# Kernel optimization log

Measured on AMD Instinct MI355X. Metric: run time of the kernel, lower is better.

Reference implementation:

```python
import jax, jax.numpy as jnp
import numpy as np

B, S = 2, 2048
DIM_IN, DIM_OUT, NUM_HEADS, DIM_QK = 1024, 128, 16, 128


def setup_inputs() -> dict:
    key = jax.random.key(0)
    k0, k1, k2, k3 = jax.random.split(key, 4)
    x = jax.random.normal(k0, (B, S, DIM_IN), jnp.float32)
    mask = jax.random.bernoulli(k1, 0.1, (B, S))  # True = masked-out token
    # xavier-normal-ish scales (exact init values are irrelevant for correctness)
    std_in = float(np.sqrt(2.0 / (NUM_HEADS * DIM_QK + DIM_IN * DIM_QK)))
    proj_in = jax.random.normal(k2, (DIM_IN, NUM_HEADS, 2 * DIM_QK + DIM_OUT), jnp.float32) * std_in
    v_bias = jnp.zeros((NUM_HEADS, DIM_OUT), jnp.float32)
    std_out = float(np.sqrt(2.0 / (DIM_OUT * DIM_OUT + NUM_HEADS * DIM_OUT)))
    proj_out = jax.random.normal(k3, (NUM_HEADS, DIM_OUT, DIM_OUT), jnp.float32) * std_out
    proj_out_bias = jnp.zeros((DIM_OUT,), jnp.float32)
    return {"x": x, "mask": mask, "proj_in": proj_in, "v_bias": v_bias,
            "proj_out": proj_out, "proj_out_bias": proj_out_bias}


def _rotary(t):
    # t: [z, s, h, d]; GPT-NeoX style rotary as in the torch Rotary module
    d = t.shape[-1]
    half = -(-d // 2)  # ceil(d/2), matches torch.arange(0,-1,-2/d)
    freq_half = 10000.0 ** (jnp.arange(half, dtype=jnp.float32) * (-2.0 / d))
    freq = jnp.concatenate([freq_half, freq_half[: half - d % 2]])  # length d
    pos = jnp.arange(t.shape[1], dtype=jnp.float32)
    ang = pos[:, None] * freq[None, :]             # [s, d]
    cos = jnp.cos(ang)[None, :, None, :]
    sin = jnp.sin(ang)[None, :, None, :]
    x1, x2 = jnp.split(t, 2, axis=-1)
    rot = jnp.concatenate([-x2, x1], axis=-1)
    return t * cos + rot * sin


def _inf_cube(t):
    return t ** 3


def reference(x, mask, proj_in, v_bias, proj_out, proj_out_bias):
    qkv = jnp.einsum('zki,iho->zkho', x, proj_in)
    q, k, v = jnp.split(qkv, [DIM_QK, 2 * DIM_QK], axis=-1)
    q = _rotary(q)
    k = _rotary(k)
    scores = jnp.einsum('zqha,zkha->zqkh', q, k) / jnp.sqrt(jnp.float32(DIM_QK))
    # dual mask: row (query) OR column (key) masked -> -inf
    m = jnp.logical_or(mask[:, :, None, None], mask[:, None, :, None])  # [z,q,k,1]
    scores = jnp.where(m, -jnp.inf, scores)
    attn = jnp.nan_to_num(jax.nn.softmax(scores, axis=2))  # softmax over k; nan rows -> 0
    o = jnp.einsum('zqkh,zkhx->zqhx', attn, v + v_bias[None, None])
    out = jnp.einsum('zqhx,hxy->zqy', _inf_cube(o), proj_out) + proj_out_bias[None, None]
    return _inf_cube(out)
```

## Files before the change

kernel.cpp:

```cpp
#include <hip/hip_runtime.h>
#include <math.h>

#define BZ 2
#define SQ 2048
#define DIN 1024
#define HH 16
#define NT 6144
#define MROWS 4096
#define KOUT 2048
#define KSPLIT 8

typedef unsigned short u16t;
typedef unsigned int u32t;
typedef __attribute__((ext_vector_type(8))) short bf16x8;
typedef __attribute__((ext_vector_type(4))) float f32x4;

__device__ __forceinline__ float cubef(float x) { return x * x * x; }

__device__ __forceinline__ u16t f2bf(float f) {
    u32t b = __float_as_uint(f);
    b += 0x7FFFu + ((b >> 16) & 1u);
    return (u16t)(b >> 16);
}
__device__ __forceinline__ float bf2f(u16t u) { return __uint_as_float(((u32t)u) << 16); }
__device__ __forceinline__ u32t pk2(float a, float b) {
    return (u32t)f2bf(a) | ((u32t)f2bf(b) << 16);
}

#if __has_builtin(__builtin_amdgcn_exp2f)
#define EXP2(x) __builtin_amdgcn_exp2f(x)
#else
#define EXP2(x) exp2f(x)
#endif

__device__ __forceinline__ void load_lds16(const void* g, void* l) {
    __builtin_amdgcn_global_load_lds((const __attribute__((address_space(1))) void*)g,
                                     (__attribute__((address_space(3))) void*)l, 16, 0, 0);
}

__global__ __launch_bounds__(256) void prep_all(const float* __restrict__ x,
                                                u16t* __restrict__ xb,
                                                float* __restrict__ tab,
                                                const float* __restrict__ W,
                                                u16t* __restrict__ Th) {
    __shared__ float tile[64][68];
    const int bx = blockIdx.x;
    const int t = threadIdx.x;

    if (bx < 2048) {
        const size_t idx = ((size_t)bx * 256 + t) * 8;
        float4 f0 = *(const float4*)&x[idx];
        float4 f1 = *(const float4*)&x[idx + 4];
        u32t h[4];
        h[0] = pk2(f0.x, f0.y); h[1] = pk2(f0.z, f0.w);
        h[2] = pk2(f1.x, f1.y); h[3] = pk2(f1.z, f1.w);
        *(uint4*)&xb[idx] = *(uint4*)&h[0];
    } else if (bx < 2560) {
        const int idx = (bx - 2048) * 256 + t;
        const int s = idx >> 6, d = idx & 63;
        float f = expf(-0.14391156831212788f * (float)d);
        float sn, cs;
        sincosf((float)s * f, &sn, &cs);
        ((float2*)tab)[idx] = make_float2(cs, sn);
    } else {
        const int idx = bx - 2560;
        const int n0 = (idx % 96) * 64;
        const int k0 = (idx / 96) * 64;
        {
            const int r = t >> 4, c = (t & 15) * 4;
            #pragma unroll
            for (int p = 0; p < 4; p++) {
                float4 v = *(const float4*)&W[(size_t)(k0 + r + p * 16) * NT + n0 + c];
                *(float4*)&tile[r + p * 16][c] = v;
            }
        }
        __syncthreads();
        const int nr = t >> 2;
        const int kc = (t & 3) * 16;
        u32t hi[8];
        #pragma unroll
        for (int j = 0; j < 8; j++)
            hi[j] = pk2(tile[kc + 2 * j][nr], tile[kc + 2 * j + 1][nr]);
        size_t ob = (size_t)(n0 + nr) * DIN + k0 + kc;
        *(uint4*)&Th[ob]     = *(uint4*)&hi[0];
        *(uint4*)&Th[ob + 8] = *(uint4*)&hi[4];
    }
}

__global__ __launch_bounds__(256) void transpose_w2(const float* __restrict__ W,
                                                    u16t* __restrict__ Th) {
    __shared__ float tile[64][68];
    const int n0 = blockIdx.x * 64;
    const int k0 = blockIdx.y * 64;
    const int t = threadIdx.x;
    {
        const int r = t >> 4, c = (t & 15) * 4;
        #pragma unroll
        for (int p = 0; p < 4; p++) {
            float4 v = *(const float4*)&W[(size_t)(k0 + r + p * 16) * 128 + n0 + c];
            *(float4*)&tile[r + p * 16][c] = v;
        }
    }
    __syncthreads();
    const int nr = t >> 2;
    const int kc = (t & 3) * 16;
    u32t hi[8];
    #pragma unroll
    for (int j = 0; j < 8; j++)
        hi[j] = pk2(tile[kc + 2 * j][nr], tile[kc + 2 * j + 1][nr]);
    size_t ob = (size_t)(n0 + nr) * KOUT + k0 + kc;
    *(uint4*)&Th[ob]     = *(uint4*)&hi[0];
    *(uint4*)&Th[ob + 8] = *(uint4*)&hi[4];
}

#define QSC 0.12751744f

__global__ __launch_bounds__(256) void gemm_qkv9(const u16t* __restrict__ Ah,
                                                 const u16t* __restrict__ Bh,
                                                 const float* __restrict__ vb,
                                                 const float* __restrict__ ropetab,
                                                 u16t* __restrict__ QB,
                                                 u16t* __restrict__ KB,
                                                 u16t* __restrict__ VTh) {
    __shared__ __align__(16) u16t smem[17408];

    const int t = threadIdx.x;
    const int lane = t & 63, wid = t >> 6;
    const int quad = lane >> 4, l15 = lane & 15;
    const int wm = (wid & 1) * 64;
    const int wn = (wid >> 1) * 64;

    const int f = blockIdx.y * 48 + blockIdx.x;
    const int L = (f & 7) * 192 + (f >> 3);
    const int rect = L / 48, rrem = L - rect * 48;
    const int tileI = (rect & 7) * 6 + rrem % 6;
    const int rowIdx = (rect >> 3) * 8 + rrem / 6;
    const int h = tileI / 3, t3 = tileI - h * 3;
    const int colBase = tileI * 128;
    const int rowBase = rowIdx * 128;
    const int sm = t & 127;
    const int skh = t >> 7;

    f32x4 acc[4][4];
    #pragma unroll
    for (int i = 0; i < 4; i++)
        #pragma unroll
        for (int j = 0; j < 4; j++) acc[i][j] = (f32x4){0.f, 0.f, 0.f, 0.f};

    const u16t* aPtr = Ah + (size_t)(rowBase + sm) * DIN + skh * 16;
    const u16t* bPtr = Bh + (size_t)(colBase + sm) * DIN + skh * 16;
    const int swoff = skh * 2048 + sm * 8;

    uint4 a0 = *(const uint4*)(aPtr);
    uint4 a1 = *(const uint4*)(aPtr + 8);
    uint4 b0 = *(const uint4*)(bPtr);
    uint4 b1 = *(const uint4*)(bPtr + 8);

    for (int it = 0; it < 32; it++) {
        const int buf = it & 1;
        const int ab = buf * 4096, bb_ = 8192 + buf * 4096;
        *(uint4*)(&smem[ab + swoff])         = a0;
        *(uint4*)(&smem[ab + swoff + 1024])  = a1;
        *(uint4*)(&smem[bb_ + swoff])        = b0;
        *(uint4*)(&smem[bb_ + swoff + 1024]) = b1;
        __syncthreads();
        {
            const int k0 = (it < 31) ? (it + 1) * 32 : it * 32;
            a0 = *(const uint4*)(aPtr + k0);
            a1 = *(const uint4*)(aPtr + k0 + 8);
            b0 = *(const uint4*)(bPtr + k0);
            b1 = *(const uint4*)(bPtr + k0 + 8);
        }
        bf16x8 ah[4], bh[4];
        #pragma unroll
        for (int mt = 0; mt < 4; mt++)
            ah[mt] = *(const bf16x8*)&smem[ab + quad * 1024 + (wm + mt * 16 + l15) * 8];
        #pragma unroll
        for (int nt = 0; nt < 4; nt++)
            bh[nt] = *(const bf16x8*)&smem[bb_ + quad * 1024 + (wn + nt * 16 + l15) * 8];
        __builtin_amdgcn_s_setprio(1);
        #pragma unroll
        for (int mt = 0; mt < 4; mt++)
            #pragma unroll
            for (int nt = 0; nt < 4; nt++)
                acc[mt][nt] = __builtin_amdgcn_mfma_f32_16x16x32_bf16(ah[mt], bh[nt], acc[mt][nt], 0, 0, 0);
        __builtin_amdgcn_s_setprio(0);
    }
    __syncthreads();

    const int z = rowBase >> 11;
    const int s0local = rowBase & 2047;
    const size_t zh = (size_t)(z * 16 + h);
    u16t* tl = smem;

    if (t3 == 2) {
        #pragma unroll
        for (int nt = 0; nt < 4; nt++) {
            float bbv = vb[h * 128 + wn + nt * 16 + l15];
            #pragma unroll
            for (int mt = 0; mt < 4; mt++)
                #pragma unroll
                for (int r = 0; r < 4; r++)
                    tl[(wm + mt * 16 + quad * 4 + r) * 136 + wn + nt * 16 + l15] =
                        f2bf(acc[mt][nt][r] + bbv);
        }
    } else {
        #pragma unroll
        for (int nt = 0; nt < 4; nt++)
            #pragma unroll
            for (int mt = 0; mt < 4; mt++)
                #pragma unroll
                for (int r = 0; r < 4; r++)
                    tl[(wm + mt * 16 + quad * 4 + r) * 136 + wn + nt * 16 + l15] =
                        f2bf(acc[mt][nt][r]);
    }
    __syncthreads();

    if (t3 != 2) {
        u16t* dstQK = (t3 ? KB : QB) + zh * 262144;
        const float sc = t3 ? 1.0f : QSC;
        const int rr = t >> 2;
        const int ch = (t & 3) << 4;
        #pragma unroll
        for (int half = 0; half < 2; half++) {
            const int row = rr + half * 64;
            const int s = s0local + row;
            const u16t* trow = &tl[row * 136];
            uint4 X1  = *(const uint4*)&trow[ch];
            uint4 X1b = *(const uint4*)&trow[ch + 8];
            uint4 X2  = *(const uint4*)&trow[ch + 64];
            uint4 X2b = *(const uint4*)&trow[ch + 72];
            u32t A_[8] = {X1.x, X1.y, X1.z, X1.w, X1b.x, X1b.y, X1b.z, X1b.w};
            u32t B_[8] = {X2.x, X2.y, X2.z, X2.w, X2b.x, X2b.y, X2b.z, X2b.w};
            u32t OA[8], OB[8];
            const float4* tb = (const float4*)&ropetab[(size_t)s * 128 + ch * 2];
            #pragma unroll
            for (int p = 0; p < 8; p++) {
                float4 tt = tb[p];
                float cs0 = tt.x * sc, sn0 = tt.y * sc;
                float cs1 = tt.z * sc, sn1 = tt.w * sc;
                float x1a = bf2f((u16t)(A_[p] & 0xFFFFu)), x1b = bf2f((u16t)(A_[p] >> 16));
                float x2a = bf2f((u16t)(B_[p] & 0xFFFFu)), x2b = bf2f((u16t)(B_[p] >> 16));
                OA[p] = pk2(x1a * cs0 - x2a * sn0, x1b * cs1 - x2b * sn1);
                OB[p] = pk2(x2a * cs0 + x1a * sn0, x2b * cs1 + x1b * sn1);
            }
            u16t* d0 = dstQK + (size_t)s * 128 + ch;
            *(uint4*)d0        = make_uint4(OA[0], OA[1], OA[2], OA[3]);
            *(uint4*)(d0 + 8)  = make_uint4(OA[4], OA[5], OA[6], OA[7]);
            *(uint4*)(d0 + 64) = make_uint4(OB[0], OB[1], OB[2], OB[3]);
            *(uint4*)(d0 + 72) = make_uint4(OB[4], OB[5], OB[6], OB[7]);
        }
    } else {
        u16t* dstV = VTh + zh * 262144 + (size_t)(s0local >> 5) * 4096;
        const int d = t & 127;
        const int g0 = t >> 7;
        #pragma unroll
        for (int gg = 0; gg < 2; gg++) {
            const int g = g0 + 2 * gg;
            const u16t* col = &tl[(g * 32) * 136 + d];
            u32t H[16];
            #pragma unroll
            for (int m = 0; m < 16; m++) {
                u32t lo = col[m * 136];
                u32t hi = col[(m + 16) * 136];
                H[m] = lo | (hi << 16);
            }
            u16t* dv = dstV + (size_t)g * 4096 + d * 32;
            *(uint4*)&dv[0]  = *(uint4*)&H[0];
            *(uint4*)&dv[8]  = *(uint4*)&H[4];
            *(uint4*)&dv[16] = *(uint4*)&H[8];
            *(uint4*)&dv[24] = *(uint4*)&H[12];
        }
    }
}

__global__ __launch_bounds__(256, 2) void attn_kernel9(const u16t* __restrict__ QB,
                                                       const u16t* __restrict__ KB,
                                                       const u16t* __restrict__ VTh,
                                                       const int* __restrict__ mask,
                                                       u16t* __restrict__ O3b) {
    const int blk = blockIdx.x;
    const int qt = blk & 15;
    const int h  = (blk >> 4) & 15;
    const int z  = blk >> 8;
    const int t  = threadIdx.x;
    const int lane = t & 63, wid = t >> 6;
    const int quad = lane >> 4, l15 = lane & 15;

    __shared__ __align__(16) u16t ks[2][32 * 136];
    __shared__ __align__(16) u16t vth[2][128 * 40];
    __shared__ __align__(16) u16t wlb[128 * 40];
    __shared__ int km[2][32];

    const int q0 = qt * 128;
    const size_t zh = (size_t)(z * 16 + h);
    const u16t* qb  = QB  + zh * 262144;
    const u16t* kb  = KB  + zh * 262144;
    const u16t* vhg = VTh + zh * 262144;

    bf16x8 qf[2][4];
    #pragma unroll
    for (int i = 0; i < 2; i++)
        #pragma unroll
        for (int kk = 0; kk < 4; kk++)
            qf[i][kk] = *(const bf16x8*)(qb + (size_t)(q0 + 16 * (2 * wid + i) + l15) * 128 + kk * 32 + quad * 8);

    int4 qm4[2];
    #pragma unroll
    for (int i = 0; i < 2; i++)
        qm4[i] = *(const int4*)&mask[z * SQ + q0 + 16 * (2 * wid + i) + 4 * quad];
    const int qmr[2][4] = {{qm4[0].x, qm4[0].y, qm4[0].z, qm4[0].w},
                           {qm4[1].x, qm4[1].y, qm4[1].z, qm4[1].w}};
    int rowoff[2];
    #pragma unroll
    for (int i = 0; i < 2; i++) rowoff[i] = (16 * (2 * wid + i) + 4 * quad) * 40;

    const int srow = t >> 3, sco = (t & 7) * 16;
    const int sdd = t >> 1, sk0 = (t & 1) * 16;

    uint4 ka, kb2, va, vb2;
    int kmv = 0;
    {
        ka  = *(const uint4*)(kb + t * 16);
        kb2 = *(const uint4*)(kb + t * 16 + 8);
        va  = *(const uint4*)(vhg + t * 16);
        vb2 = *(const uint4*)(vhg + t * 16 + 8);
        if (t < 32) kmv = mask[z * SQ + t];
    }

    f32x4 acc[2][8];
    #pragma unroll
    for (int i = 0; i < 2; i++)
        #pragma unroll
        for (int d = 0; d < 8; d++) acc[i][d] = (f32x4){0.f, 0.f, 0.f, 0.f};
    float dsum[2][4] = {{0.f, 0.f, 0.f, 0.f}, {0.f, 0.f, 0.f, 0.f}};

    for (int it = 0; it < 64; it++) {
        const int buf = it & 1;
        *(uint4*)&ks[buf][srow * 136 + sco]     = ka;
        *(uint4*)&ks[buf][srow * 136 + sco + 8] = kb2;
        *(uint4*)&vth[buf][sdd * 40 + sk0]      = va;
        *(uint4*)&vth[buf][sdd * 40 + sk0 + 8]  = vb2;
        if (t < 32) km[buf][t] = kmv;

        __syncthreads();

        {
            const int ktn = (it < 63) ? (it + 1) * 32 : it * 32;
            const u16t* src = kb + (size_t)ktn * 128 + t * 16;
            ka  = *(const uint4*)(src);
            kb2 = *(const uint4*)(src + 8);
            const u16t* srch = vhg + (size_t)(ktn >> 5) * 4096 + t * 16;
            va  = *(const uint4*)(srch);
            vb2 = *(const uint4*)(srch + 8);
            if (t < 32) kmv = mask[z * SQ + ktn + t];
        }

        f32x4 s4[2][2];
        #pragma unroll
        for (int i = 0; i < 2; i++)
            #pragma unroll
            for (int n = 0; n < 2; n++) s4[i][n] = (f32x4){0.f, 0.f, 0.f, 0.f};
        __builtin_amdgcn_s_setprio(1);
        #pragma unroll
        for (int kk = 0; kk < 4; kk++) {
            bf16x8 kf0 = *(const bf16x8*)&ks[buf][l15 * 136 + kk * 32 + quad * 8];
            bf16x8 kf1 = *(const bf16x8*)&ks[buf][(16 + l15) * 136 + kk * 32 + quad * 8];
            s4[0][0] = __builtin_amdgcn_mfma_f32_16x16x32_bf16(qf[0][kk], kf0, s4[0][0], 0, 0, 0);
            s4[0][1] = __builtin_amdgcn_mfma_f32_16x16x32_bf16(qf[0][kk], kf1, s4[0][1], 0, 0, 0);
            s4[1][0] = __builtin_amdgcn_mfma_f32_16x16x32_bf16(qf[1][kk], kf0, s4[1][0], 0, 0, 0);
            s4[1][1] = __builtin_amdgcn_mfma_f32_16x16x32_bf16(qf[1][kk], kf1, s4[1][1], 0, 0, 0);
        }
        __builtin_amdgcn_s_setprio(0);
        {
            int colm0 = km[buf][l15], colm1 = km[buf][16 + l15];
            #pragma unroll
            for (int i = 0; i < 2; i++)
                #pragma unroll
                for (int r = 0; r < 4; r++) {
                    float w0 = colm0 ? 0.f : EXP2(s4[i][0][r]);
                    float w1 = colm1 ? 0.f : EXP2(s4[i][1][r]);
                    dsum[i][r] += w0 + w1;
                    u32t pkw;
                    asm("v_cvt_pk_bf16_f32 %0, %1, %2" : "=v"(pkw) : "v"(w0), "v"(w1));
                    *(u32t*)&wlb[rowoff[i] + r * 40 + 2 * l15] = pkw;
                }
        }
        bf16x8 pa[2];
        #pragma unroll
        for (int i = 0; i < 2; i++)
            pa[i] = *(const bf16x8*)&wlb[(16 * (2 * wid + i) + l15) * 40 + quad * 8];
        __builtin_amdgcn_s_setprio(1);
        #pragma unroll
        for (int dt = 0; dt < 8; dt++) {
            bf16x8 vh = *(const bf16x8*)&vth[buf][(16 * dt + l15) * 40 + quad * 8];
            acc[0][dt] = __builtin_amdgcn_mfma_f32_16x16x32_bf16(pa[0], vh, acc[0][dt], 0, 0, 0);
            acc[1][dt] = __builtin_amdgcn_mfma_f32_16x16x32_bf16(pa[1], vh, acc[1][dt], 0, 0, 0);
        }
        __builtin_amdgcn_s_setprio(0);
    }

    #pragma unroll
    for (int i = 0; i < 2; i++)
        #pragma unroll
        for (int r = 0; r < 4; r++) {
            float v = dsum[i][r];
            v += __shfl_xor(v, 1);
            v += __shfl_xor(v, 2);
            v += __shfl_xor(v, 4);
            v += __shfl_xor(v, 8);
            dsum[i][r] = v;
        }

    #pragma unroll
    for (int i = 0; i < 2; i++)
        #pragma unroll
        for (int r = 0; r < 4; r++) {
            int row = 16 * (2 * wid + i) + 4 * quad + r;
            float inv = (qmr[i][r] || !(dsum[i][r] > 0.f)) ? 0.f : 1.f / dsum[i][r];
            u16t* dst = O3b + (size_t)(z * SQ + q0 + row) * KOUT + h * 128;
            #pragma unroll
            for (int dt = 0; dt < 8; dt++)
                dst[16 * dt + l15] = f2bf(cubef(acc[i][dt][r] * inv));
        }
}

#define GQ_WAITBAR(N) do {                                                 \
    asm volatile("s_waitcnt vmcnt(" #N ")" ::: "memory");                  \
    __builtin_amdgcn_s_barrier();                                          \
    __builtin_amdgcn_sched_barrier(0);                                     \
} while (0)

#define GQ_STAGE(TI) do {                                                  \
    const int _k0 = (TI) * 32;                                             \
    const int _bb = ((TI) & 3) * 8192;                                     \
    load_lds16(aPtr + _k0,     &smem[_bb + wbase]);                        \
    load_lds16(aPtr + _k0 + 8, &smem[_bb + wbase + 1024]);                 \
    load_lds16(bPtr + _k0,     &smem[_bb + 4096 + wbase]);                 \
    load_lds16(bPtr + _k0 + 8, &smem[_bb + 4096 + wbase + 1024]);          \
} while (0)

#define GQ_COMPUTE(TI) do {                                                \
    const int _bb = ((TI) & 3) * 8192;                                     \
    bf16x8 ah[4], bh[4];                                                   \
    _Pragma("unroll")                                                      \
    for (int mt = 0; mt < 4; mt++)                                         \
        ah[mt] = *(const bf16x8*)&smem[_bb + quad * 1024 + (wm + mt * 16 + l15) * 8]; \
    _Pragma("unroll")                                                      \
    for (int nt = 0; nt < 4; nt++)                                         \
        bh[nt] = *(const bf16x8*)&smem[_bb + 4096 + quad * 1024 + (wn + nt * 16 + l15) * 8]; \
    __builtin_amdgcn_s_setprio(1);                                         \
    _Pragma("unroll")                                                      \
    for (int mt = 0; mt < 4; mt++)                                         \
        _Pragma("unroll")                                                  \
        for (int nt = 0; nt < 4; nt++)                                     \
            acc[mt][nt] = __builtin_amdgcn_mfma_f32_16x16x32_bf16(ah[mt], bh[nt], acc[mt][nt], 0, 0, 0); \
    __builtin_amdgcn_s_setprio(0);                                         \
} while (0)

__global__ __launch_bounds__(256, 2) void final_gemm4(const u16t* __restrict__ Ab,
                                                      const u16t* __restrict__ Bh,
                                                      float* __restrict__ part) {
    __shared__ __align__(16) u16t smem[32768];

    const int t = threadIdx.x;
    const int lane = t & 63, wid = t >> 6;
    const int quad = lane >> 4, l15 = lane & 15;
    const int wm = (wid & 1) * 64;
    const int wn = (wid >> 1) * 64;
    const int rowBase = blockIdx.x * 128;
    const int kBase   = blockIdx.y * (KOUT / KSPLIT);
    const int sm = t & 127;
    const int skh = t >> 7;

    f32x4 acc[4][4];
    #pragma unroll
    for (int i = 0; i < 4; i++)
        #pragma unroll
        for (int j = 0; j < 4; j++) acc[i][j] = (f32x4){0.f, 0.f, 0.f, 0.f};

    const u16t* aPtr = Ab + (size_t)(rowBase + sm) * KOUT + kBase + skh * 16;
    const u16t* bPtr = Bh + (size_t)sm * KOUT + kBase + skh * 16;
    const int wbase = (wid >> 1) * 2048 + (wid & 1) * 512;

    GQ_STAGE(0);
    GQ_STAGE(1);
    for (int i = 0; i < 6; i++) {
        GQ_STAGE(i + 2);
        GQ_WAITBAR(8);
        GQ_COMPUTE(i);
    }
    GQ_WAITBAR(4);
    GQ_COMPUTE(6);
    GQ_WAITBAR(0);
    GQ_COMPUTE(7);

    float* pbase = part + (size_t)blockIdx.y * ((size_t)MROWS * 128);
    #pragma unroll
    for (int mt = 0; mt < 4; mt++)
        #pragma unroll
        for (int nt = 0; nt < 4; nt++) {
            int col = wn + nt * 16 + l15;
            #pragma unroll
            for (int r = 0; r < 4; r++) {
                int row = rowBase + wm + mt * 16 + quad * 4 + r;
                pbase[(size_t)row * 128 + col] = acc[mt][nt][r];
            }
        }
}

__global__ __launch_bounds__(256) void reduce_bias_cube(const float* __restrict__ part,
                                                        const float* __restrict__ bias,
                                                        float* __restrict__ out) {
    const int idx = (blockIdx.x * 256 + threadIdx.x) * 4;
    float4 s = {0.f, 0.f, 0.f, 0.f};
    #pragma unroll
    for (int p = 0; p < KSPLIT; p++) {
        float4 v = *(const float4*)&part[(size_t)p * ((size_t)MROWS * 128) + idx];
        s.x += v.x; s.y += v.y; s.z += v.z; s.w += v.w;
    }
    float4 b = *(const float4*)&bias[idx & 127];
    float4 r;
    r.x = cubef(s.x + b.x);
    r.y = cubef(s.y + b.y);
    r.z = cubef(s.z + b.z);
    r.w = cubef(s.w + b.w);
    *(float4*)&out[idx] = r;
}

extern "C" void kernel_launch(void* const* d_in, const int* in_sizes, int n_in,
                              void* d_out, int out_size, void* d_ws, size_t ws_size,
                              hipStream_t stream) {
    const float* x        = (const float*)d_in[0];
    const int*   mask     = (const int*)d_in[1];
    const float* proj_in  = (const float*)d_in[2];
    const float* v_bias   = (const float*)d_in[3];
    const float* proj_out = (const float*)d_in[4];
    const float* po_bias  = (const float*)d_in[5];
    float* out = (float*)d_out;

    u16t* QB  = (u16t*)d_ws;
    u16t* KB  = QB + (size_t)8388608;
    u16t* VTh = KB + (size_t)8388608;
    u16t* xb  = VTh + (size_t)8388608;
    u16t* O3b = xb + (size_t)4194304;
    u16t* pTh = O3b;
    float* ropetab = (float*)(O3b + (size_t)6291456);
    u16t* WTh = QB;
    float* partials = (float*)(WTh + (size_t)128 * KOUT);

    prep_all<<<2048 + 512 + 1536, 256, 0, stream>>>(x, xb, ropetab, proj_in, pTh);
    gemm_qkv9<<<dim3(48, 32), 256, 0, stream>>>(xb, pTh, v_bias, ropetab, QB, KB, VTh);
    attn_kernel9<<<BZ * HH * (SQ / 128), 256, 0, stream>>>(QB, KB, VTh, mask, O3b);
    transpose_w2<<<dim3(2, KOUT / 64), 256, 0, stream>>>(proj_out, WTh);
    final_gemm4<<<dim3(MROWS / 128, KSPLIT), 256, 0, stream>>>(O3b, WTh, partials);
    reduce_bias_cube<<<(MROWS * 128) / (256 * 4), 256, 0, stream>>>(partials, po_bias, out);
}
```

Measured before the change: 295.6 us.

## Load attention K/V fragments directly from global memory and remap blocks per XCD

The attention kernel stops staging K and V tiles through double-buffered shared memory with per-tile barriers. Each wave now reads its MFMA operand fragments for K, V and the column mask straight from global memory, relying on L2 for reuse across waves and blocks. Block indices are also remapped so that all query tiles of a (batch, head) pair land on the same XCD, which should improve L2 locality. Separately, the s_setprio hints around the MFMA loops in both GEMM kernels are removed. Dropping the barriers and LDS traffic comes at the cost of redundant, less coalesced global loads whose latency is exposed inside the loop.

```diff
diff --git a/kernel.cpp b/kernel.cpp
--- a/kernel.cpp
+++ b/kernel.cpp
@@ -32,11 +32,6 @@
 #else
 #define EXP2(x) exp2f(x)
 #endif
-
-__device__ __forceinline__ void load_lds16(const void* g, void* l) {
-    __builtin_amdgcn_global_load_lds((const __attribute__((address_space(1))) void*)g,
-                                     (__attribute__((address_space(3))) void*)l, 16, 0, 0);
-}
 
 __global__ __launch_bounds__(256) void prep_all(const float* __restrict__ x,
                                                 u16t* __restrict__ xb,
@@ -115,13 +110,13 @@
 
 #define QSC 0.12751744f
 
-__global__ __launch_bounds__(256) void gemm_qkv9(const u16t* __restrict__ Ah,
-                                                 const u16t* __restrict__ Bh,
-                                                 const float* __restrict__ vb,
-                                                 const float* __restrict__ ropetab,
-                                                 u16t* __restrict__ QB,
-                                                 u16t* __restrict__ KB,
-                                                 u16t* __restrict__ VTh) {
+__global__ __launch_bounds__(256) void gemm_qkv11(const u16t* __restrict__ Ah,
+                                                  const u16t* __restrict__ Bh,
+                                                  const float* __restrict__ vb,
+                                                  const float* __restrict__ ropetab,
+                                                  u16t* __restrict__ QB,
+                                                  u16t* __restrict__ KB,
+                                                  u16t* __restrict__ VTh) {
     __shared__ __align__(16) u16t smem[17408];
 
     const int t = threadIdx.x;
@@ -178,13 +173,11 @@
         #pragma unroll
         for (int nt = 0; nt < 4; nt++)
             bh[nt] = *(const bf16x8*)&smem[bb_ + quad * 1024 + (wn + nt * 16 + l15) * 8];
-        __builtin_amdgcn_s_setprio(1);
         #pragma unroll
         for (int mt = 0; mt < 4; mt++)
             #pragma unroll
             for (int nt = 0; nt < 4; nt++)
                 acc[mt][nt] = __builtin_amdgcn_mfma_f32_16x16x32_bf16(ah[mt], bh[nt], acc[mt][nt], 0, 0, 0);
-        __builtin_amdgcn_s_setprio(0);
     }
     __syncthreads();
 
@@ -274,29 +267,27 @@
     }
 }
 
-__global__ __launch_bounds__(256, 2) void attn_kernel9(const u16t* __restrict__ QB,
-                                                       const u16t* __restrict__ KB,
-                                                       const u16t* __restrict__ VTh,
-                                                       const int* __restrict__ mask,
-                                                       u16t* __restrict__ O3b) {
+__global__ __launch_bounds__(256, 2) void attn_kernel11(const u16t* __restrict__ QB,
+                                                        const u16t* __restrict__ KB,
+                                                        const u16t* __restrict__ VTh,
+                                                        const int* __restrict__ mask,
+                                                        u16t* __restrict__ O3b) {
     const int blk = blockIdx.x;
-    const int qt = blk & 15;
-    const int h  = (blk >> 4) & 15;
-    const int z  = blk >> 8;
+    const int xcd = blk & 7, loc = blk >> 3;
+    const int zh = xcd * 4 + (loc >> 4);
+    const int qt = loc & 15;
+    const int z = zh >> 4, h = zh & 15;
     const int t  = threadIdx.x;
     const int lane = t & 63, wid = t >> 6;
     const int quad = lane >> 4, l15 = lane & 15;
 
-    __shared__ __align__(16) u16t ks[2][32 * 136];
-    __shared__ __align__(16) u16t vth[2][128 * 40];
     __shared__ __align__(16) u16t wlb[128 * 40];
-    __shared__ int km[2][32];
 
     const int q0 = qt * 128;
-    const size_t zh = (size_t)(z * 16 + h);
-    const u16t* qb  = QB  + zh * 262144;
-    const u16t* kb  = KB  + zh * 262144;
-    const u16t* vhg = VTh + zh * 262144;
+    const u16t* qb  = QB  + (size_t)zh * 262144;
+    const u16t* kbg = KB  + (size_t)zh * 262144;
+    const u16t* vhg = VTh + (size_t)zh * 262144;
+    const int mb = z * SQ;
 
     bf16x8 qf[2][4];
     #pragma unroll
@@ -308,26 +299,13 @@
     int4 qm4[2];
     #pragma unroll
     for (int i = 0; i < 2; i++)
-        qm4[i] = *(const int4*)&mask[z * SQ + q0 + 16 * (2 * wid + i) + 4 * quad];
+        qm4[i] = *(const int4*)&mask[mb + q0 + 16 * (2 * wid + i) + 4 * quad];
     const int qmr[2][4] = {{qm4[0].x, qm4[0].y, qm4[0].z, qm4[0].w},
                            {qm4[1].x, qm4[1].y, qm4[1].z, qm4[1].w}};
     int rowoff[2];
     #pragma unroll
     for (int i = 0; i < 2; i++) rowoff[i] = (16 * (2 * wid + i) + 4 * quad) * 40;
 
-    const int srow = t >> 3, sco = (t & 7) * 16;
-    const int sdd = t >> 1, sk0 = (t & 1) * 16;
-
-    uint4 ka, kb2, va, vb2;
-    int kmv = 0;
-    {
-        ka  = *(const uint4*)(kb + t * 16);
-        kb2 = *(const uint4*)(kb + t * 16 + 8);
-        va  = *(const uint4*)(vhg + t * 16);
-        vb2 = *(const uint4*)(vhg + t * 16 + 8);
-        if (t < 32) kmv = mask[z * SQ + t];
-    }
-
     f32x4 acc[2][8];
     #pragma unroll
     for (int i = 0; i < 2; i++)
@@ -335,26 +313,16 @@
         for (int d = 0; d < 8; d++) acc[i][d] = (f32x4){0.f, 0.f, 0.f, 0.f};
     float dsum[2][4] = {{0.f, 0.f, 0.f, 0.f}, {0.f, 0.f, 0.f, 0.f}};
 
-    for (int it = 0; it < 64; it++) {
-        const int buf = it & 1;
-        *(uint4*)&ks[buf][srow * 136 + sco]     = ka;
-        *(uint4*)&ks[buf][srow * 136 + sco + 8] = kb2;
-        *(uint4*)&vth[buf][sdd * 40 + sk0]      = va;
-        *(uint4*)&vth[buf][sdd * 40 + sk0 + 8]  = vb2;
-        if (t < 32) km[buf][t] = kmv;
-
-        __syncthreads();
-
-        {
-            const int ktn = (it < 63) ? (it + 1) * 32 : it * 32;
-            const u16t* src = kb + (size_t)ktn * 128 + t * 16;
-            ka  = *(const uint4*)(src);
-            kb2 = *(const uint4*)(src + 8);
-            const u16t* srch = vhg + (size_t)(ktn >> 5) * 4096 + t * 16;
-            va  = *(const uint4*)(srch);
-            vb2 = *(const uint4*)(srch + 8);
-            if (t < 32) kmv = mask[z * SQ + ktn + t];
-        }
+    for (int kt = 0; kt < 64; kt++) {
+        const u16t* kb0 = kbg + (size_t)kt * 4096;
+        bf16x8 kf0[4], kf1[4];
+        #pragma unroll
+        for (int kk = 0; kk < 4; kk++) {
+            kf0[kk] = *(const bf16x8*)(kb0 + l15 * 128 + kk * 32 + quad * 8);
+            kf1[kk] = *(const bf16x8*)(kb0 + (16 + l15) * 128 + kk * 32 + quad * 8);
+        }
+        const int colm0 = mask[mb + kt * 32 + l15];
+        const int colm1 = mask[mb + kt * 32 + 16 + l15];
 
         f32x4 s4[2][2];
         #pragma unroll
@@ -364,16 +332,13 @@
         __builtin_amdgcn_s_setprio(1);
         #pragma unroll
         for (int kk = 0; kk < 4; kk++) {
-            bf16x8 kf0 = *(const bf16x8*)&ks[buf][l15 * 136 + kk * 32 + quad * 8];
-            bf16x8 kf1 = *(const bf16x8*)&ks[buf][(16 + l15) * 136 + kk * 32 + quad * 8];
-            s4[0][0] = __builtin_amdgcn_mfma_f32_16x16x32_bf16(qf[0][kk], kf0, s4[0][0], 0, 0, 0);
-            s4[0][1] = __builtin_amdgcn_mfma_f32_16x16x32_bf16(qf[0][kk], kf1, s4[0][1], 0, 0, 0);
-            s4[1][0] = __builtin_amdgcn_mfma_f32_16x16x32_bf16(qf[1][kk], kf0, s4[1][0], 0, 0, 0);
-            s4[1][1] = __builtin_amdgcn_mfma_f32_16x16x32_bf16(qf[1][kk], kf1, s4[1][1], 0, 0, 0);
+            s4[0][0] = __builtin_amdgcn_mfma_f32_16x16x32_bf16(qf[0][kk], kf0[kk], s4[0][0], 0, 0, 0);
+            s4[0][1] = __builtin_amdgcn_mfma_f32_16x16x32_bf16(qf[0][kk], kf1[kk], s4[0][1], 0, 0, 0);
+            s4[1][0] = __builtin_amdgcn_mfma_f32_16x16x32_bf16(qf[1][kk], kf0[kk], s4[1][0], 0, 0, 0);
+            s4[1][1] = __builtin_amdgcn_mfma_f32_16x16x32_bf16(qf[1][kk], kf1[kk], s4[1][1], 0, 0, 0);
         }
         __builtin_amdgcn_s_setprio(0);
         {
-            int colm0 = km[buf][l15], colm1 = km[buf][16 + l15];
             #pragma unroll
             for (int i = 0; i < 2; i++)
                 #pragma unroll
@@ -390,10 +355,11 @@
         #pragma unroll
         for (int i = 0; i < 2; i++)
             pa[i] = *(const bf16x8*)&wlb[(16 * (2 * wid + i) + l15) * 40 + quad * 8];
+        const u16t* vb0 = vhg + (size_t)kt * 4096;
         __builtin_amdgcn_s_setprio(1);
         #pragma unroll
         for (int dt = 0; dt < 8; dt++) {
-            bf16x8 vh = *(const bf16x8*)&vth[buf][(16 * dt + l15) * 40 + quad * 8];
+            bf16x8 vh = *(const bf16x8*)(vb0 + (16 * dt + l15) * 32 + quad * 8);
             acc[0][dt] = __builtin_amdgcn_mfma_f32_16x16x32_bf16(pa[0], vh, acc[0][dt], 0, 0, 0);
             acc[1][dt] = __builtin_amdgcn_mfma_f32_16x16x32_bf16(pa[1], vh, acc[1][dt], 0, 0, 0);
         }
@@ -423,6 +389,11 @@
             for (int dt = 0; dt < 8; dt++)
                 dst[16 * dt + l15] = f2bf(cubef(acc[i][dt][r] * inv));
         }
+}
+
+__device__ __forceinline__ void load_lds16(const void* g, void* l) {
+    __builtin_amdgcn_global_load_lds((const __attribute__((address_space(1))) void*)g,
+                                     (__attribute__((address_space(3))) void*)l, 16, 0, 0);
 }
 
 #define GQ_WAITBAR(N) do {                                                 \
@@ -449,13 +420,11 @@
     _Pragma("unroll")                                                      \
     for (int nt = 0; nt < 4; nt++)                                         \
         bh[nt] = *(const bf16x8*)&smem[_bb + 4096 + quad * 1024 + (wn + nt * 16 + l15) * 8]; \
-    __builtin_amdgcn_s_setprio(1);                                         \
     _Pragma("unroll")                                                      \
     for (int mt = 0; mt < 4; mt++)                                         \
         _Pragma("unroll")                                                  \
         for (int nt = 0; nt < 4; nt++)                                     \
             acc[mt][nt] = __builtin_amdgcn_mfma_f32_16x16x32_bf16(ah[mt], bh[nt], acc[mt][nt], 0, 0, 0); \
-    __builtin_amdgcn_s_setprio(0);                                         \
 } while (0)
 
 __global__ __launch_bounds__(256, 2) void final_gemm4(const u16t* __restrict__ Ab,
@@ -550,8 +519,8 @@
     float* partials = (float*)(WTh + (size_t)128 * KOUT);
 
     prep_all<<<2048 + 512 + 1536, 256, 0, stream>>>(x, xb, ropetab, proj_in, pTh);
-    gemm_qkv9<<<dim3(48, 32), 256, 0, stream>>>(xb, pTh, v_bias, ropetab, QB, KB, VTh);
-    attn_kernel9<<<BZ * HH * (SQ / 128), 256, 0, stream>>>(QB, KB, VTh, mask, O3b);
+    gemm_qkv11<<<dim3(48, 32), 256, 0, stream>>>(xb, pTh, v_bias, ropetab, QB, KB, VTh);
+    attn_kernel11<<<BZ * HH * (SQ / 128), 256, 0, stream>>>(QB, KB, VTh, mask, O3b);
     transpose_w2<<<dim3(2, KOUT / 64), 256, 0, stream>>>(proj_out, WTh);
     final_gemm4<<<dim3(MROWS / 128, KSPLIT), 256, 0, stream>>>(O3b, WTh, partials);
     reduce_bias_cube<<<(MROWS * 128) / (256 * 4), 256, 0, stream>>>(partials, po_bias, out);
```

After: 395.1 us. 1.34x slower.

## Double attention query tile per block, remap blocks to XCDs, drop setprio

Applied to the files above, without the earlier changes.

Each attention block now handles 256 query rows (four 16-row tiles per wave) instead of 128, so every K/V tile staged in LDS is reused by twice as many queries. The grid drops to 256 blocks, and the block index is remapped so that all query tiles of a (batch, head) pair land on the same XCD for better L2 locality on K/V. Launch bounds change to one block per SM to leave room for the larger accumulators. The s_setprio hints are also removed from the QKV GEMM, attention and final GEMM inner loops. The risks are lower occupancy, higher register pressure, and only 256 blocks to fill the device.

```diff
diff --git a/kernel.cpp b/kernel.cpp
--- a/kernel.cpp
+++ b/kernel.cpp
@@ -115,13 +115,13 @@
 
 #define QSC 0.12751744f
 
-__global__ __launch_bounds__(256) void gemm_qkv9(const u16t* __restrict__ Ah,
-                                                 const u16t* __restrict__ Bh,
-                                                 const float* __restrict__ vb,
-                                                 const float* __restrict__ ropetab,
-                                                 u16t* __restrict__ QB,
-                                                 u16t* __restrict__ KB,
-                                                 u16t* __restrict__ VTh) {
+__global__ __launch_bounds__(256) void gemm_qkv11(const u16t* __restrict__ Ah,
+                                                  const u16t* __restrict__ Bh,
+                                                  const float* __restrict__ vb,
+                                                  const float* __restrict__ ropetab,
+                                                  u16t* __restrict__ QB,
+                                                  u16t* __restrict__ KB,
+                                                  u16t* __restrict__ VTh) {
     __shared__ __align__(16) u16t smem[17408];
 
     const int t = threadIdx.x;
@@ -178,13 +178,11 @@
         #pragma unroll
         for (int nt = 0; nt < 4; nt++)
             bh[nt] = *(const bf16x8*)&smem[bb_ + quad * 1024 + (wn + nt * 16 + l15) * 8];
-        __builtin_amdgcn_s_setprio(1);
         #pragma unroll
         for (int mt = 0; mt < 4; mt++)
             #pragma unroll
             for (int nt = 0; nt < 4; nt++)
                 acc[mt][nt] = __builtin_amdgcn_mfma_f32_16x16x32_bf16(ah[mt], bh[nt], acc[mt][nt], 0, 0, 0);
-        __builtin_amdgcn_s_setprio(0);
     }
     __syncthreads();
 
@@ -274,46 +272,49 @@
     }
 }
 
-__global__ __launch_bounds__(256, 2) void attn_kernel9(const u16t* __restrict__ QB,
-                                                       const u16t* __restrict__ KB,
-                                                       const u16t* __restrict__ VTh,
-                                                       const int* __restrict__ mask,
-                                                       u16t* __restrict__ O3b) {
+__global__ __launch_bounds__(256, 1) void attn_kernel12(const u16t* __restrict__ QB,
+                                                        const u16t* __restrict__ KB,
+                                                        const u16t* __restrict__ VTh,
+                                                        const int* __restrict__ mask,
+                                                        u16t* __restrict__ O3b) {
     const int blk = blockIdx.x;
-    const int qt = blk & 15;
-    const int h  = (blk >> 4) & 15;
-    const int z  = blk >> 8;
+    const int xcd = blk & 7, loc = blk >> 3;
+    const int zh = xcd * 4 + (loc >> 3);
+    const int qt = loc & 7;
+    const int z = zh >> 4, h = zh & 15;
     const int t  = threadIdx.x;
     const int lane = t & 63, wid = t >> 6;
     const int quad = lane >> 4, l15 = lane & 15;
 
     __shared__ __align__(16) u16t ks[2][32 * 136];
     __shared__ __align__(16) u16t vth[2][128 * 40];
-    __shared__ __align__(16) u16t wlb[128 * 40];
+    __shared__ __align__(16) u16t wlb[256 * 40];
     __shared__ int km[2][32];
 
-    const int q0 = qt * 128;
-    const size_t zh = (size_t)(z * 16 + h);
-    const u16t* qb  = QB  + zh * 262144;
-    const u16t* kb  = KB  + zh * 262144;
-    const u16t* vhg = VTh + zh * 262144;
-
-    bf16x8 qf[2][4];
-    #pragma unroll
-    for (int i = 0; i < 2; i++)
+    const int q0 = qt * 256;
+    const u16t* qb  = QB  + (size_t)zh * 262144;
+    const u16t* kb  = KB  + (size_t)zh * 262144;
+    const u16t* vhg = VTh + (size_t)zh * 262144;
+    const int mb = z * SQ;
+
+    bf16x8 qf[4][4];
+    #pragma unroll
+    for (int i = 0; i < 4; i++)
         #pragma unroll
         for (int kk = 0; kk < 4; kk++)
-            qf[i][kk] = *(const bf16x8*)(qb + (size_t)(q0 + 16 * (2 * wid + i) + l15) * 128 + kk * 32 + quad * 8);
-
-    int4 qm4[2];
-    #pragma unroll
-    for (int i = 0; i < 2; i++)
-        qm4[i] = *(const int4*)&mask[z * SQ + q0 + 16 * (2 * wid + i) + 4 * quad];
-    const int qmr[2][4] = {{qm4[0].x, qm4[0].y, qm4[0].z, qm4[0].w},
-                           {qm4[1].x, qm4[1].y, qm4[1].z, qm4[1].w}};
-    int rowoff[2];
-    #pragma unroll
-    for (int i = 0; i < 2; i++) rowoff[i] = (16 * (2 * wid + i) + 4 * quad) * 40;
+            qf[i][kk] = *(const bf16x8*)(qb + (size_t)(q0 + 16 * (4 * wid + i) + l15) * 128 + kk * 32 + quad * 8);
+
+    int4 qm4[4];
+    #pragma unroll
+    for (int i = 0; i < 4; i++)
+        qm4[i] = *(const int4*)&mask[mb + q0 + 16 * (4 * wid + i) + 4 * quad];
+    const int qmr[4][4] = {{qm4[0].x, qm4[0].y, qm4[0].z, qm4[0].w},
+                           {qm4[1].x, qm4[1].y, qm4[1].z, qm4[1].w},
+                           {qm4[2].x, qm4[2].y, qm4[2].z, qm4[2].w},
+                           {qm4[3].x, qm4[3].y, qm4[3].z, qm4[3].w}};
+    int rowoff[4];
+    #pragma unroll
+    for (int i = 0; i < 4; i++) rowoff[i] = (16 * (4 * wid + i) + 4 * quad) * 40;
 
     const int srow = t >> 3, sco = (t & 7) * 16;
     const int sdd = t >> 1, sk0 = (t & 1) * 16;
@@ -325,15 +326,19 @@
         kb2 = *(const uint4*)(kb + t * 16 + 8);
         va  = *(const uint4*)(vhg + t * 16);
         vb2 = *(const uint4*)(vhg + t * 16 + 8);
-        if (t < 32) kmv = mask[z * SQ + t];
-    }
-
-    f32x4 acc[2][8];
-    #pragma unroll
-    for (int i = 0; i < 2; i++)
+        if (t < 32) kmv = mask[mb + t];
+    }
+
+    f32x4 acc[4][8];
+    #pragma unroll
+    for (int i = 0; i < 4; i++)
         #pragma unroll
         for (int d = 0; d < 8; d++) acc[i][d] = (f32x4){0.f, 0.f, 0.f, 0.f};
-    float dsum[2][4] = {{0.f, 0.f, 0.f, 0.f}, {0.f, 0.f, 0.f, 0.f}};
+    float dsum[4][4];
+    #pragma unroll
+    for (int i = 0; i < 4; i++)
+        #pragma unroll
+        for (int r = 0; r < 4; r++) dsum[i][r] = 0.f;
 
     for (int it = 0; it < 64; it++) {
         const int buf = it & 1;
@@ -353,29 +358,28 @@
             const u16t* srch = vhg + (size_t)(ktn >> 5) * 4096 + t * 16;
             va  = *(const uint4*)(srch);
             vb2 = *(const uint4*)(srch + 8);
-            if (t < 32) kmv = mask[z * SQ + ktn + t];
-        }
-
-        f32x4 s4[2][2];
-        #pragma unroll
-        for (int i = 0; i < 2; i++)
+            if (t < 32) kmv = mask[mb + ktn + t];
+        }
+
+        f32x4 s4[4][2];
+        #pragma unroll
+        for (int i = 0; i < 4; i++)
             #pragma unroll
             for (int n = 0; n < 2; n++) s4[i][n] = (f32x4){0.f, 0.f, 0.f, 0.f};
-        __builtin_amdgcn_s_setprio(1);
         #pragma unroll
         for (int kk = 0; kk < 4; kk++) {
             bf16x8 kf0 = *(const bf16x8*)&ks[buf][l15 * 136 + kk * 32 + quad * 8];
             bf16x8 kf1 = *(const bf16x8*)&ks[buf][(16 + l15) * 136 + kk * 32 + quad * 8];
-            s4[0][0] = __builtin_amdgcn_mfma_f32_16x16x32_bf16(qf[0][kk], kf0, s4[0][0], 0, 0, 0);
-            s4[0][1] = __builtin_amdgcn_mfma_f32_16x16x32_bf16(qf[0][kk], kf1, s4[0][1], 0, 0, 0);
-            s4[1][0] = __builtin_amdgcn_mfma_f32_16x16x32_bf16(qf[1][kk], kf0, s4[1][0], 0, 0, 0);
-            s4[1][1] = __builtin_amdgcn_mfma_f32_16x16x32_bf16(qf[1][kk], kf1, s4[1][1], 0, 0, 0);
-        }
-        __builtin_amdgcn_s_setprio(0);
+            #pragma unroll
+            for (int i = 0; i < 4; i++) {
+                s4[i][0] = __builtin_amdgcn_mfma_f32_16x16x32_bf16(qf[i][kk], kf0, s4[i][0], 0, 0, 0);
+                s4[i][1] = __builtin_amdgcn_mfma_f32_16x16x32_bf16(qf[i][kk], kf1, s4[i][1], 0, 0, 0);
+            }
+        }
         {
             int colm0 = km[buf][l15], colm1 = km[buf][16 + l15];
             #pragma unroll
-            for (int i = 0; i < 2; i++)
+            for (int i = 0; i < 4; i++)
                 #pragma unroll
                 for (int r = 0; r < 4; r++) {
                     float w0 = colm0 ? 0.f : EXP2(s4[i][0][r]);
@@ -386,22 +390,21 @@
                     *(u32t*)&wlb[rowoff[i] + r * 40 + 2 * l15] = pkw;
                 }
         }
-        bf16x8 pa[2];
-        #pragma unroll
-        for (int i = 0; i < 2; i++)
-            pa[i] = *(const bf16x8*)&wlb[(16 * (2 * wid + i) + l15) * 40 + quad * 8];
-        __builtin_amdgcn_s_setprio(1);
+        bf16x8 pa[4];
+        #pragma unroll
+        for (int i = 0; i < 4; i++)
+            pa[i] = *(const bf16x8*)&wlb[(16 * (4 * wid + i) + l15) * 40 + quad * 8];
         #pragma unroll
         for (int dt = 0; dt < 8; dt++) {
             bf16x8 vh = *(const bf16x8*)&vth[buf][(16 * dt + l15) * 40 + quad * 8];
-            acc[0][dt] = __builtin_amdgcn_mfma_f32_16x16x32_bf16(pa[0], vh, acc[0][dt], 0, 0, 0);
-            acc[1][dt] = __builtin_amdgcn_mfma_f32_16x16x32_bf16(pa[1], vh, acc[1][dt], 0, 0, 0);
-        }
-        __builtin_amdgcn_s_setprio(0);
-    }
-
-    #pragma unroll
-    for (int i = 0; i < 2; i++)
+            #pragma unroll
+            for (int i = 0; i < 4; i++)
+                acc[i][dt] = __builtin_amdgcn_mfma_f32_16x16x32_bf16(pa[i], vh, acc[i][dt], 0, 0, 0);
+        }
+    }
+
+    #pragma unroll
+    for (int i = 0; i < 4; i++)
         #pragma unroll
         for (int r = 0; r < 4; r++) {
             float v = dsum[i][r];
@@ -413,10 +416,10 @@
         }
 
     #pragma unroll
-    for (int i = 0; i < 2; i++)
+    for (int i = 0; i < 4; i++)
         #pragma unroll
         for (int r = 0; r < 4; r++) {
-            int row = 16 * (2 * wid + i) + 4 * quad + r;
+            int row = 16 * (4 * wid + i) + 4 * quad + r;
             float inv = (qmr[i][r] || !(dsum[i][r] > 0.f)) ? 0.f : 1.f / dsum[i][r];
             u16t* dst = O3b + (size_t)(z * SQ + q0 + row) * KOUT + h * 128;
             #pragma unroll
@@ -449,13 +452,11 @@
     _Pragma("unroll")                                                      \
     for (int nt = 0; nt < 4; nt++)                                         \
         bh[nt] = *(const bf16x8*)&smem[_bb + 4096 + quad * 1024 + (wn + nt * 16 + l15) * 8]; \
-    __builtin_amdgcn_s_setprio(1);                                         \
     _Pragma("unroll")                                                      \
     for (int mt = 0; mt < 4; mt++)                                         \
         _Pragma("unroll")                                                  \
         for (int nt = 0; nt < 4; nt++)                                     \
             acc[mt][nt] = __builtin_amdgcn_mfma_f32_16x16x32_bf16(ah[mt], bh[nt], acc[mt][nt], 0, 0, 0); \
-    __builtin_amdgcn_s_setprio(0);                                         \
 } while (0)
 
 __global__ __launch_bounds__(256, 2) void final_gemm4(const u16t* __restrict__ Ab,
@@ -550,8 +551,8 @@
     float* partials = (float*)(WTh + (size_t)128 * KOUT);
 
     prep_all<<<2048 + 512 + 1536, 256, 0, stream>>>(x, xb, ropetab, proj_in, pTh);
-    gemm_qkv9<<<dim3(48, 32), 256, 0, stream>>>(xb, pTh, v_bias, ropetab, QB, KB, VTh);
-    attn_kernel9<<<BZ * HH * (SQ / 128), 256, 0, stream>>>(QB, KB, VTh, mask, O3b);
+    gemm_qkv11<<<dim3(48, 32), 256, 0, stream>>>(xb, pTh, v_bias, ropetab, QB, KB, VTh);
+    attn_kernel12<<<256, 256, 0, stream>>>(QB, KB, VTh, mask, O3b);
     transpose_w2<<<dim3(2, KOUT / 64), 256, 0, stream>>>(proj_out, WTh);
     final_gemm4<<<dim3(MROWS / 128, KSPLIT), 256, 0, stream>>>(O3b, WTh, partials);
     reduce_bias_cube<<<(MROWS * 128) / (256 * 4), 256, 0, stream>>>(partials, po_bias, out);
```

Result: slower. 314.2 us (+6.3%).
